# Kernel optimization log

Measured on AMD Instinct MI355X. Metric: run time of the kernel, lower is better.

Reference implementation:

```python
import jax, jax.numpy as jnp
import numpy as np

N_NODES = 100000
N_EDGES = 1600000
IN_DIM = 128
OUT_DIM = 64


def setup_inputs() -> dict:
    key = jax.random.key(0)
    k1, k2, k3, k4, k5 = jax.random.split(key, 5)
    x = jax.random.normal(k1, (N_NODES, IN_DIM), dtype=jnp.float32)
    src = jax.random.randint(k2, (N_EDGES,), 0, N_NODES)
    dst = jax.random.randint(k3, (N_EDGES,), 0, N_NODES)
    edge_index = jnp.stack([src, dst]).astype(jnp.int64)
    # Glorot-ish init scale for the two GCN weight matrices (bias=False)
    W1 = jax.random.normal(k4, (IN_DIM, OUT_DIM), dtype=jnp.float32) / np.sqrt(IN_DIM)
    W2 = jax.random.normal(k5, (OUT_DIM, OUT_DIM), dtype=jnp.float32) / np.sqrt(OUT_DIM)
    return {"x": x, "edge_index": edge_index, "W1": W1, "W2": W2}


def _gcn_conv(h, W, src, dst, dinv_sqrt, n_nodes):
    """PyG GCNConv (bias=False): out[i] = sum_{j->i} d_j^-1/2 d_i^-1/2 (h_j @ W),
    with self-loops already folded into (src, dst, dinv_sqrt)."""
    h = h @ W                                    # [N, out]
    norm = dinv_sqrt[src] * dinv_sqrt[dst]       # [E+N]
    msg = h[src] * norm[:, None]                 # gather + scale, [E+N, out]
    return jax.ops.segment_sum(msg, dst, num_segments=n_nodes)


def reference(x, edge_index, W1, W2):
    n = x.shape[0]
    # add self-loops (static shape: E + N edges)
    loop = jnp.arange(n, dtype=edge_index.dtype)
    src = jnp.concatenate([edge_index[0], loop])
    dst = jnp.concatenate([edge_index[1], loop])
    # symmetric normalization degrees (in-degree over dst, unit edge weights)
    deg = jax.ops.segment_sum(jnp.ones_like(dst, dtype=x.dtype), dst, num_segments=n)
    dinv_sqrt = jax.lax.rsqrt(deg)  # deg >= 1 because of self-loops
    # dropout is identity in eval mode (training=False)
    h = _gcn_conv(x, W1, src, dst, dinv_sqrt, n)
    h = jax.nn.relu(h)
    out = _gcn_conv(h, W2, src, dst, dinv_sqrt, n)
    return out
```

## Files before the change

### kernel.cpp

```cpp
#include <hip/hip_runtime.h>
#include <hip/hip_bf16.h>

#define IN_DIM  128
#define OUT_DIM 64
#define EPB 4096
#define NBK_MAX 512

typedef short  bf16x8 __attribute__((ext_vector_type(8)));
typedef float  f32x4  __attribute__((ext_vector_type(4)));
typedef unsigned long long u64;

__device__ __forceinline__ unsigned short f2bf(float f) {
    unsigned u = __float_as_uint(f);
    u += 0x7fffu + ((u >> 16) & 1u);
    return (unsigned short)(u >> 16);
}
__device__ __forceinline__ float bf2f(unsigned short h) {
    return __uint_as_float((unsigned)h << 16);
}


__global__ __launch_bounds__(256) void k_cnt(const int* __restrict__ dst,
                                             unsigned* __restrict__ colcnt,
                                             int nE, int nbk, int nblk) {
    __shared__ unsigned h[NBK_MAX];
    for (int b = threadIdx.x; b < NBK_MAX; b += 256) h[b] = 0u;
    __syncthreads();
    int blk = blockIdx.x;
    int e0 = blk * EPB, e1 = min(e0 + EPB, nE);
    for (int e = e0 + threadIdx.x; e < e1; e += 256)
        atomicAdd(&h[dst[e] >> 8], 1u);
    __syncthreads();
    for (int b = threadIdx.x; b < nbk; b += 256)
        colcnt[(size_t)b * nblk + blk] = h[b];
}

__global__ __launch_bounds__(512) void k_bsum(unsigned* __restrict__ colcnt,
                                              unsigned* __restrict__ btot,
                                              int nbk, int nblk) {
    __shared__ unsigned s[512];
    int b = blockIdx.x;
    unsigned v = (threadIdx.x < (unsigned)nblk) ? colcnt[(size_t)b * nblk + threadIdx.x] : 0u;
    s[threadIdx.x] = v;
    __syncthreads();
    for (int d = 1; d < 512; d <<= 1) {
        unsigned t = (threadIdx.x >= (unsigned)d) ? s[threadIdx.x - d] : 0u;
        __syncthreads();
        s[threadIdx.x] += t;
        __syncthreads();
    }
    if (threadIdx.x < (unsigned)nblk)
        colcnt[(size_t)b * nblk + threadIdx.x] = s[threadIdx.x] - v;
    if (threadIdx.x == 511) btot[b] = s[511];
}

__global__ __launch_bounds__(512) void k_btots(const unsigned* __restrict__ btot,
                                               unsigned* __restrict__ bbase,
                                               int nbk, int nE) {
    __shared__ unsigned s[512];
    unsigned v = (threadIdx.x < (unsigned)nbk) ? btot[threadIdx.x] : 0u;
    s[threadIdx.x] = v;
    __syncthreads();
    for (int d = 1; d < 512; d <<= 1) {
        unsigned t = (threadIdx.x >= (unsigned)d) ? s[threadIdx.x - d] : 0u;
        __syncthreads();
        s[threadIdx.x] += t;
        __syncthreads();
    }
    if (threadIdx.x < (unsigned)nbk) bbase[threadIdx.x] = s[threadIdx.x] - v;
    if (threadIdx.x == 0) bbase[nbk] = (unsigned)nE;
}

__global__ __launch_bounds__(256) void k_part(const int* __restrict__ src,
                                              const int* __restrict__ dst,
                                              const unsigned* __restrict__ colcnt,
                                              const unsigned* __restrict__ bbase,
                                              u64* __restrict__ ebuf,
                                              int nE, int nbk, int nblk) {
    __shared__ unsigned curs[NBK_MAX];
    int blk = blockIdx.x;
    for (int b = threadIdx.x; b < nbk; b += 256)
        curs[b] = bbase[b] + colcnt[(size_t)b * nblk + blk];
    __syncthreads();
    int e0 = blk * EPB, e1 = min(e0 + EPB, nE);
    for (int e = e0 + threadIdx.x; e < e1; e += 256) {
        int d = dst[e], s = src[e];
        unsigned p = atomicAdd(&curs[d >> 8], 1u);
        ebuf[p] = ((u64)(unsigned)d << 32) | (unsigned)s;
    }
}

__global__ __launch_bounds__(256) void k_fine(const u64* __restrict__ ebuf,
                                              const unsigned* __restrict__ bbase,
                                              unsigned* __restrict__ offs,
                                              float* __restrict__ dinv,
                                              int* __restrict__ perm, int n) {
    __shared__ unsigned deg[256], pos[256], cur[256];
    int b = blockIdx.x;
    int node0 = b << 8;
    unsigned ebeg = bbase[b], eend = bbase[b + 1];
    deg[threadIdx.x] = 0u;
    __syncthreads();
    for (unsigned e = ebeg + threadIdx.x; e < eend; e += 256) {
        u64 rec = ebuf[e];
        atomicAdd(&deg[(unsigned)(rec >> 32) & 255u], 1u);
    }
    __syncthreads();
    unsigned v = deg[threadIdx.x];
    pos[threadIdx.x] = v;
    __syncthreads();
    for (int d = 1; d < 256; d <<= 1) {
        unsigned t = (threadIdx.x >= (unsigned)d) ? pos[threadIdx.x - d] : 0u;
        __syncthreads();
        pos[threadIdx.x] += t;
        __syncthreads();
    }
    unsigned excl = pos[threadIdx.x] - v;
    cur[threadIdx.x] = excl;
    int node = node0 + threadIdx.x;
    if (node < n) {
        offs[node] = ebeg + excl;
        dinv[node] = rsqrtf((float)v + 1.0f);
    }
    __syncthreads();
    for (unsigned e = ebeg + threadIdx.x; e < eend; e += 256) {
        u64 rec = ebuf[e];
        unsigned p = atomicAdd(&cur[(unsigned)(rec >> 32) & 255u], 1u);
        perm[ebeg + p] = (int)(unsigned)rec;
    }
}

template <int KD, bool RELU>
__global__ __launch_bounds__(256) void k_linm(const float* __restrict__ in,
                                              const float* __restrict__ W,
                                              const float* __restrict__ dinv,
                                              unsigned short* __restrict__ outp, int n) {
    constexpr int LDK = KD + 8;
    __shared__ unsigned short WH[64 * LDK];
    __shared__ unsigned short WL[64 * LDK];
    for (int i = threadIdx.x; i < KD * 64; i += 256) {
        int k = i >> 6, c = i & 63;
        float wv = W[i];
        unsigned short h = f2bf(wv);
        WH[c * LDK + k] = h;
        WL[c * LDK + k] = f2bf(wv - bf2f(h));
    }
    __syncthreads();

    int wid = threadIdx.x >> 6, lane = threadIdx.x & 63;
    int r0 = blockIdx.x * 64 + wid * 16;

    constexpr int NK = KD / 32;
    int arow = r0 + (lane & 15);
    int ar = arow < n ? arow : (n - 1);
    int k8 = (lane >> 4) * 8;

    bf16x8 ah[NK], al[NK];
    {
        const float* rp = in + (size_t)ar * KD;
        float dvin = RELU ? dinv[ar] : 0.f;
#pragma unroll
        for (int ks = 0; ks < NK; ++ks) {
            float4 v0 = *(const float4*)(rp + ks * 32 + k8);
            float4 v1 = *(const float4*)(rp + ks * 32 + k8 + 4);
            float xv[8] = {v0.x, v0.y, v0.z, v0.w, v1.x, v1.y, v1.z, v1.w};
#pragma unroll
            for (int j = 0; j < 8; ++j) {
                float f = xv[j];
                if (RELU) f = fmaxf(dvin * f, 0.f);
                unsigned short h = f2bf(f);
                ah[ks][j] = (short)h;
                al[ks][j] = (short)f2bf(f - bf2f(h));
            }
        }
    }

    f32x4 acc[4];
#pragma unroll
    for (int nt = 0; nt < 4; ++nt) {
        int col = nt * 16 + (lane & 15);
        const unsigned short* bh = &WH[col * LDK + k8];
        const unsigned short* bl = &WL[col * LDK + k8];
        f32x4 a = {0.f, 0.f, 0.f, 0.f};
#pragma unroll
        for (int ks = 0; ks < NK; ++ks) {
            bf16x8 Bh = *(const bf16x8*)(bh + ks * 32);
            bf16x8 Bl = *(const bf16x8*)(bl + ks * 32);
            a = __builtin_amdgcn_mfma_f32_16x16x32_bf16(ah[ks], Bh, a, 0, 0, 0);
            a = __builtin_amdgcn_mfma_f32_16x16x32_bf16(ah[ks], Bl, a, 0, 0, 0);
            a = __builtin_amdgcn_mfma_f32_16x16x32_bf16(al[ks], Bh, a, 0, 0, 0);
        }
        acc[nt] = a;
    }

    int orow0 = r0 + (lane >> 4) * 4;
#pragma unroll
    for (int j = 0; j < 4; ++j) {
        int row = orow0 + j;
        if (row < n) {
            float dv = dinv[row];
#pragma unroll
            for (int nt = 0; nt < 4; ++nt)
                outp[(size_t)row * 64 + nt * 16 + (lane & 15)] = f2bf(dv * acc[nt][j]);
        }
    }
}

template <bool FIN>
__global__ __launch_bounds__(256) void k_gather(const unsigned short* __restrict__ hs,
                                                const unsigned* __restrict__ offs,
                                                const int* __restrict__ perm,
                                                const float* __restrict__ dinv,
                                                float* __restrict__ outb,
                                                int n, int nE) {
    int lane = threadIdx.x & 63;
    int g = lane >> 4, li = lane & 15;
    int r = blockIdx.x * 4 + (threadIdx.x >> 6);
    if (r >= n) return;
    unsigned beg = offs[r];
    unsigned end = (r + 1 < n) ? offs[r + 1] : (unsigned)nE;

    float4 a0 = {0.f, 0.f, 0.f, 0.f}, a1 = a0, a2 = a0, a3 = a0;
    if (g == 0) {
        ushort4 sv = *(const ushort4*)(hs + (size_t)r * 64 + li * 4);
        a0.x = bf2f(sv.x); a0.y = bf2f(sv.y); a0.z = bf2f(sv.z); a0.w = bf2f(sv.w);
    }

    for (unsigned e0 = beg; e0 < end; e0 += 64) {
        unsigned c = min(64u, end - e0);
        int sl = (lane < (int)c) ? perm[e0 + lane] : 0;
        unsigned k = 0;
        for (; k + 16 <= c; k += 16) {
            int s0 = __shfl(sl, (int)(k + g));
            int s1 = __shfl(sl, (int)(k + 4 + g));
            int s2 = __shfl(sl, (int)(k + 8 + g));
            int s3 = __shfl(sl, (int)(k + 12 + g));
            ushort4 v0 = *(const ushort4*)(hs + (size_t)s0 * 64 + li * 4);
            ushort4 v1 = *(const ushort4*)(hs + (size_t)s1 * 64 + li * 4);
            ushort4 v2 = *(const ushort4*)(hs + (size_t)s2 * 64 + li * 4);
            ushort4 v3 = *(const ushort4*)(hs + (size_t)s3 * 64 + li * 4);
            a0.x += bf2f(v0.x); a0.y += bf2f(v0.y); a0.z += bf2f(v0.z); a0.w += bf2f(v0.w);
            a1.x += bf2f(v1.x); a1.y += bf2f(v1.y); a1.z += bf2f(v1.z); a1.w += bf2f(v1.w);
            a2.x += bf2f(v2.x); a2.y += bf2f(v2.y); a2.z += bf2f(v2.z); a2.w += bf2f(v2.w);
            a3.x += bf2f(v3.x); a3.y += bf2f(v3.y); a3.z += bf2f(v3.z); a3.w += bf2f(v3.w);
        }
        for (; k < c; k += 4) {
            int idx = (int)k + g;
            bool val = idx < (int)c;
            int s = __shfl(sl, val ? idx : 0);
            ushort4 v = *(const ushort4*)(hs + (size_t)s * 64 + li * 4);
            if (val) {
                a0.x += bf2f(v.x); a0.y += bf2f(v.y);
                a0.z += bf2f(v.z); a0.w += bf2f(v.w);
            }
        }
    }

    float4 acc;
    acc.x = (a0.x + a1.x) + (a2.x + a3.x);
    acc.y = (a0.y + a1.y) + (a2.y + a3.y);
    acc.z = (a0.z + a1.z) + (a2.z + a3.z);
    acc.w = (a0.w + a1.w) + (a2.w + a3.w);
    acc.x += __shfl_xor(acc.x, 16); acc.x += __shfl_xor(acc.x, 32);
    acc.y += __shfl_xor(acc.y, 16); acc.y += __shfl_xor(acc.y, 32);
    acc.z += __shfl_xor(acc.z, 16); acc.z += __shfl_xor(acc.z, 32);
    acc.w += __shfl_xor(acc.w, 16); acc.w += __shfl_xor(acc.w, 32);

    if (g == 0) {
        if (FIN) {
            float dv = dinv[r];
            acc.x *= dv; acc.y *= dv; acc.z *= dv; acc.w *= dv;
        }
        *(float4*)(outb + (size_t)r * 64 + li * 4) = acc;
    }
}

extern "C" void kernel_launch(void* const* d_in, const int* in_sizes, int n_in,
                              void* d_out, int out_size, void* d_ws, size_t ws_size,
                              hipStream_t stream) {
    const float* x  = (const float*)d_in[0];
    const int*   ei = (const int*)d_in[1];
    const float* W1 = (const float*)d_in[2];
    const float* W2 = (const float*)d_in[3];
    float* out = (float*)d_out;

    int n  = in_sizes[0] / IN_DIM;
    int nE = in_sizes[1] / 2;
    const int* src = ei;
    const int* dst = ei + nE;

    int nbk  = (n + 255) >> 8;
    int nblk = (nE + EPB - 1) / EPB;

    char* w = (char*)d_ws;
    size_t nAl = ((size_t)n * 4 + 255) & ~(size_t)255;
    float*          dinv   = (float*)w;     w += nAl;
    unsigned*       offs   = (unsigned*)w;  w += nAl;
    unsigned*       colcnt = (unsigned*)w;  w += ((size_t)nbk * nblk * 4 + 255) & ~(size_t)255;
    unsigned*       btot   = (unsigned*)w;  w += ((size_t)nbk * 4 + 255) & ~(size_t)255;
    unsigned*       bbase  = (unsigned*)w;  w += ((size_t)(nbk + 1) * 4 + 255) & ~(size_t)255;
    u64*            ebuf   = (u64*)w;       w += ((size_t)nE * 8 + 255) & ~(size_t)255;
    int*            perm   = (int*)w;       w += ((size_t)nE * 4 + 255) & ~(size_t)255;
    unsigned short* hs     = (unsigned short*)w; w += (size_t)n * 64 * 2;
    float*          agg    = out;

    int gRow = (n + 3) / 4;
    int gMf  = (n + 63) / 64;

    k_cnt  <<<nblk, 256, 0, stream>>>(dst, colcnt, nE, nbk, nblk);
    k_bsum <<<nbk,  512, 0, stream>>>(colcnt, btot, nbk, nblk);
    k_btots<<<1,    512, 0, stream>>>(btot, bbase, nbk, nE);
    k_part <<<nblk, 256, 0, stream>>>(src, dst, colcnt, bbase, ebuf, nE, nbk, nblk);
    k_fine <<<nbk,  256, 0, stream>>>(ebuf, bbase, offs, dinv, perm, n);

    k_linm<IN_DIM, false><<<gMf, 256, 0, stream>>>(x, W1, dinv, hs, n);
    k_gather<false><<<gRow, 256, 0, stream>>>(hs, offs, perm, dinv, agg, n, nE);

    k_linm<OUT_DIM, true><<<gMf, 256, 0, stream>>>(agg, W2, dinv, hs, n);
    k_gather<true><<<gRow, 256, 0, stream>>>(hs, offs, perm, dinv, out, n, nE);
}
```

Before: 165.1 us.

## Pack edge records into 32 bits and gather four rows per wavefront

```diff
diff --git a/kernel.cpp b/kernel.cpp
--- a/kernel.cpp
+++ b/kernel.cpp
@@ -8,7 +8,6 @@
 
 typedef short  bf16x8 __attribute__((ext_vector_type(8)));
 typedef float  f32x4  __attribute__((ext_vector_type(4)));
-typedef unsigned long long u64;
 
 __device__ __forceinline__ unsigned short f2bf(float f) {
     unsigned u = __float_as_uint(f);
@@ -75,7 +74,7 @@
                                               const int* __restrict__ dst,
                                               const unsigned* __restrict__ colcnt,
                                               const unsigned* __restrict__ bbase,
-                                              u64* __restrict__ ebuf,
+                                              unsigned* __restrict__ ebuf,
                                               int nE, int nbk, int nblk) {
     __shared__ unsigned curs[NBK_MAX];
     int blk = blockIdx.x;
@@ -86,11 +85,11 @@
     for (int e = e0 + threadIdx.x; e < e1; e += 256) {
         int d = dst[e], s = src[e];
         unsigned p = atomicAdd(&curs[d >> 8], 1u);
-        ebuf[p] = ((u64)(unsigned)d << 32) | (unsigned)s;
-    }
-}
-
-__global__ __launch_bounds__(256) void k_fine(const u64* __restrict__ ebuf,
+        ebuf[p] = ((unsigned)(d & 255) << 17) | (unsigned)s;
+    }
+}
+
+__global__ __launch_bounds__(256) void k_fine(const unsigned* __restrict__ ebuf,
                                               const unsigned* __restrict__ bbase,
                                               unsigned* __restrict__ offs,
                                               float* __restrict__ dinv,
@@ -101,10 +100,8 @@
     unsigned ebeg = bbase[b], eend = bbase[b + 1];
     deg[threadIdx.x] = 0u;
     __syncthreads();
-    for (unsigned e = ebeg + threadIdx.x; e < eend; e += 256) {
-        u64 rec = ebuf[e];
-        atomicAdd(&deg[(unsigned)(rec >> 32) & 255u], 1u);
-    }
+    for (unsigned e = ebeg + threadIdx.x; e < eend; e += 256)
+        atomicAdd(&deg[ebuf[e] >> 17], 1u);
     __syncthreads();
     unsigned v = deg[threadIdx.x];
     pos[threadIdx.x] = v;
@@ -124,9 +121,9 @@
     }
     __syncthreads();
     for (unsigned e = ebeg + threadIdx.x; e < eend; e += 256) {
-        u64 rec = ebuf[e];
-        unsigned p = atomicAdd(&cur[(unsigned)(rec >> 32) & 255u], 1u);
-        perm[ebeg + p] = (int)(unsigned)rec;
+        unsigned rec = ebuf[e];
+        unsigned p = atomicAdd(&cur[rec >> 17], 1u);
+        perm[ebeg + p] = (int)(rec & 0x1FFFFu);
     }
 }
 
@@ -215,58 +212,58 @@
                                                 int n, int nE) {
     int lane = threadIdx.x & 63;
     int g = lane >> 4, li = lane & 15;
-    int r = blockIdx.x * 4 + (threadIdx.x >> 6);
-    if (r >= n) return;
-    unsigned beg = offs[r];
-    unsigned end = (r + 1 < n) ? offs[r + 1] : (unsigned)nE;
-
-    float4 a0 = {0.f, 0.f, 0.f, 0.f}, a1 = a0, a2 = a0, a3 = a0;
-    if (g == 0) {
-        ushort4 sv = *(const ushort4*)(hs + (size_t)r * 64 + li * 4);
-        a0.x = bf2f(sv.x); a0.y = bf2f(sv.y); a0.z = bf2f(sv.z); a0.w = bf2f(sv.w);
-    }
-
-    for (unsigned e0 = beg; e0 < end; e0 += 64) {
-        unsigned c = min(64u, end - e0);
-        int sl = (lane < (int)c) ? perm[e0 + lane] : 0;
-        unsigned k = 0;
-        for (; k + 16 <= c; k += 16) {
-            int s0 = __shfl(sl, (int)(k + g));
-            int s1 = __shfl(sl, (int)(k + 4 + g));
-            int s2 = __shfl(sl, (int)(k + 8 + g));
-            int s3 = __shfl(sl, (int)(k + 12 + g));
-            ushort4 v0 = *(const ushort4*)(hs + (size_t)s0 * 64 + li * 4);
-            ushort4 v1 = *(const ushort4*)(hs + (size_t)s1 * 64 + li * 4);
-            ushort4 v2 = *(const ushort4*)(hs + (size_t)s2 * 64 + li * 4);
-            ushort4 v3 = *(const ushort4*)(hs + (size_t)s3 * 64 + li * 4);
-            a0.x += bf2f(v0.x); a0.y += bf2f(v0.y); a0.z += bf2f(v0.z); a0.w += bf2f(v0.w);
-            a1.x += bf2f(v1.x); a1.y += bf2f(v1.y); a1.z += bf2f(v1.z); a1.w += bf2f(v1.w);
-            a2.x += bf2f(v2.x); a2.y += bf2f(v2.y); a2.z += bf2f(v2.z); a2.w += bf2f(v2.w);
-            a3.x += bf2f(v3.x); a3.y += bf2f(v3.y); a3.z += bf2f(v3.z); a3.w += bf2f(v3.w);
-        }
-        for (; k < c; k += 4) {
-            int idx = (int)k + g;
-            bool val = idx < (int)c;
-            int s = __shfl(sl, val ? idx : 0);
-            ushort4 v = *(const ushort4*)(hs + (size_t)s * 64 + li * 4);
-            if (val) {
-                a0.x += bf2f(v.x); a0.y += bf2f(v.y);
-                a0.z += bf2f(v.z); a0.w += bf2f(v.w);
-            }
-        }
-    }
-
-    float4 acc;
-    acc.x = (a0.x + a1.x) + (a2.x + a3.x);
-    acc.y = (a0.y + a1.y) + (a2.y + a3.y);
-    acc.z = (a0.z + a1.z) + (a2.z + a3.z);
-    acc.w = (a0.w + a1.w) + (a2.w + a3.w);
-    acc.x += __shfl_xor(acc.x, 16); acc.x += __shfl_xor(acc.x, 32);
-    acc.y += __shfl_xor(acc.y, 16); acc.y += __shfl_xor(acc.y, 32);
-    acc.z += __shfl_xor(acc.z, 16); acc.z += __shfl_xor(acc.z, 32);
-    acc.w += __shfl_xor(acc.w, 16); acc.w += __shfl_xor(acc.w, 32);
-
-    if (g == 0) {
+    int r = (blockIdx.x * 4 + (threadIdx.x >> 6)) * 4 + g;
+    bool nvalid = r < n;
+    int rc = nvalid ? r : (n - 1);
+    unsigned beg = offs[rc];
+    unsigned end = (rc + 1 < n) ? offs[rc + 1] : (unsigned)nE;
+    unsigned deg = nvalid ? (end - beg) : 0u;
+
+    float4 q0, q1 = {0.f,0.f,0.f,0.f}, q2 = q1, q3 = q1;
+    {
+        ushort4 sv = *(const ushort4*)(hs + (size_t)rc * 64 + li * 4);
+        q0.x = bf2f(sv.x); q0.y = bf2f(sv.y); q0.z = bf2f(sv.z); q0.w = bf2f(sv.w);
+    }
+
+    unsigned m1 = max(deg, (unsigned)__shfl_xor((int)deg, 16));
+    unsigned mdeg = max(m1, (unsigned)__shfl_xor((int)m1, 32));
+
+    for (unsigned c0 = 0; c0 < mdeg; c0 += 16) {
+        int sl = 0;
+        if (c0 + li < deg) sl = perm[beg + c0 + li];
+        unsigned rem = mdeg - c0;
+        unsigned kmax = rem < 16u ? rem : 16u;
+        for (unsigned k = 0; k < kmax; k += 4) {
+            int s0 = __shfl(sl, (int)(g * 16) + (int)k);
+            int s1 = __shfl(sl, (int)(g * 16) + (int)k + 1);
+            int s2 = __shfl(sl, (int)(g * 16) + (int)k + 2);
+            int s3 = __shfl(sl, (int)(g * 16) + (int)k + 3);
+            unsigned d0 = c0 + k;
+            if (d0 < deg) {
+                ushort4 v = *(const ushort4*)(hs + (size_t)s0 * 64 + li * 4);
+                q0.x += bf2f(v.x); q0.y += bf2f(v.y); q0.z += bf2f(v.z); q0.w += bf2f(v.w);
+            }
+            if (d0 + 1 < deg) {
+                ushort4 v = *(const ushort4*)(hs + (size_t)s1 * 64 + li * 4);
+                q1.x += bf2f(v.x); q1.y += bf2f(v.y); q1.z += bf2f(v.z); q1.w += bf2f(v.w);
+            }
+            if (d0 + 2 < deg) {
+                ushort4 v = *(const ushort4*)(hs + (size_t)s2 * 64 + li * 4);
+                q2.x += bf2f(v.x); q2.y += bf2f(v.y); q2.z += bf2f(v.z); q2.w += bf2f(v.w);
+            }
+            if (d0 + 3 < deg) {
+                ushort4 v = *(const ushort4*)(hs + (size_t)s3 * 64 + li * 4);
+                q3.x += bf2f(v.x); q3.y += bf2f(v.y); q3.z += bf2f(v.z); q3.w += bf2f(v.w);
+            }
+        }
+    }
+
+    if (nvalid) {
+        float4 acc;
+        acc.x = (q0.x + q1.x) + (q2.x + q3.x);
+        acc.y = (q0.y + q1.y) + (q2.y + q3.y);
+        acc.z = (q0.z + q1.z) + (q2.z + q3.z);
+        acc.w = (q0.w + q1.w) + (q2.w + q3.w);
         if (FIN) {
             float dv = dinv[r];
             acc.x *= dv; acc.y *= dv; acc.z *= dv; acc.w *= dv;
@@ -299,12 +296,12 @@
     unsigned*       colcnt = (unsigned*)w;  w += ((size_t)nbk * nblk * 4 + 255) & ~(size_t)255;
     unsigned*       btot   = (unsigned*)w;  w += ((size_t)nbk * 4 + 255) & ~(size_t)255;
     unsigned*       bbase  = (unsigned*)w;  w += ((size_t)(nbk + 1) * 4 + 255) & ~(size_t)255;
-    u64*            ebuf   = (u64*)w;       w += ((size_t)nE * 8 + 255) & ~(size_t)255;
+    unsigned*       ebuf   = (unsigned*)w;  w += ((size_t)nE * 4 + 255) & ~(size_t)255;
     int*            perm   = (int*)w;       w += ((size_t)nE * 4 + 255) & ~(size_t)255;
     unsigned short* hs     = (unsigned short*)w; w += (size_t)n * 64 * 2;
     float*          agg    = out;
 
-    int gRow = (n + 3) / 4;
+    int gRow = (n + 15) / 16;
     int gMf  = (n + 63) / 64;
 
     k_cnt  <<<nblk, 256, 0, stream>>>(dst, colcnt, nE, nbk, nblk);
```

Measured after the change: 168.4 us. Within noise of the previous version (+2.0%).
